# Optimization experiments

Measured on AMD Instinct MI355X. Metric: run time of the kernel, lower is better.

## Reference

```python
import jax, jax.numpy as jnp
import numpy as np

B, H, N, T, E, D = 8, 8, 64, 256, 512, 64  # batch, heads, series, window, embed, feature
TAU = 1.0
DH = E // H  # per-head dim = 64


def setup_inputs() -> dict:
    key = jax.random.key(0)
    ks = jax.random.split(key, 7)
    f32 = jnp.float32
    return {
        "q": jax.random.normal(ks[0], (B, N, E), f32),
        "k": jax.random.normal(ks[1], (B, N, E), f32),
        "v": jax.random.normal(ks[2], (B, H, N, T, D), f32),
        # nn.Linear weights use torch (out, in) convention, bias=False
        "Wq": jax.random.normal(ks[3], (E, E), f32) * (E ** -0.5),
        "Wk": jax.random.normal(ks[4], (E, E), f32) * (E ** -0.5),
        # causal-convolution temporal mixing kernel per head/series
        "Wconv": jax.random.normal(ks[5], (H, N, T, T), f32) * (T ** -0.5),
        # concat projection: (out=D, in=H*D)
        "Wcat": jax.random.normal(ks[6], (D, H * D), f32) * ((H * D) ** -0.5),
    }


def reference(q, k, v, Wq, Wk, Wconv, Wcat):
    # Q/K projections, split into heads: (B,N,E) -> (B,H,N,DH)
    Q = (q @ Wq.T).reshape(B, N, H, DH).transpose(0, 2, 1, 3)
    K = (k @ Wk.T).reshape(B, N, H, DH).transpose(0, 2, 1, 3)

    # Causal convolution V projection: lower-triangular masked temporal mixing
    causal = jnp.tril(jnp.ones((T, T), v.dtype))
    V = jnp.einsum('hnts,bhnsd->bhntd', Wconv * causal, v)  # (B,H,N,T,D)

    # tau-scaled multi-head attention over the series axis
    scores = jnp.einsum('bhid,bhjd->bhij', Q, K) / (TAU * np.sqrt(DH).astype(np.float32))
    attn = jax.nn.softmax(scores, axis=-1)  # (B,H,N,N); dropout=0 (eval)
    out = jnp.einsum('bhij,bhjtd->bhitd', attn, V)  # (B,H,N,T,D)

    # reshape/permute chain == (B,H,N,T,D) -> (B,N,T,H*D)
    out = out.transpose(0, 2, 3, 1, 4).reshape(B, N, T, H * D)
    return out @ Wcat.T  # (B,N,T,D)
```

## Files before the change

kernel.cpp:

```cpp
#include <hip/hip_runtime.h>
#include <hip/hip_bf16.h>


typedef unsigned short u16;
typedef unsigned int u32;
typedef __attribute__((ext_vector_type(8))) short short8;
typedef __attribute__((ext_vector_type(4))) float f32x4;

static __device__ __forceinline__ u16 f2bf(float f) {
    u32 x; __builtin_memcpy(&x, &f, 4);
    u32 r = (x + 0x7fffu + ((x >> 16) & 1u)) >> 16;
    return (u16)r;
}
static __device__ __forceinline__ short8 pack8(float4 a, float4 b) {
    short8 r;
    r[0] = (short)f2bf(a.x); r[1] = (short)f2bf(a.y);
    r[2] = (short)f2bf(a.z); r[3] = (short)f2bf(a.w);
    r[4] = (short)f2bf(b.x); r[5] = (short)f2bf(b.y);
    r[6] = (short)f2bf(b.z); r[7] = (short)f2bf(b.w);
    return r;
}
static __device__ __forceinline__ short8 mk_bfrag(f32x4 a, f32x4 b) {
    u32 w0 = (__float_as_uint(a[0]) >> 16) | (__float_as_uint(a[1]) & 0xffff0000u);
    u32 w1 = (__float_as_uint(a[2]) >> 16) | (__float_as_uint(a[3]) & 0xffff0000u);
    u32 w2 = (__float_as_uint(b[0]) >> 16) | (__float_as_uint(b[1]) & 0xffff0000u);
    u32 w3 = (__float_as_uint(b[2]) >> 16) | (__float_as_uint(b[3]) & 0xffff0000u);
    uint4 u = make_uint4(w0, w1, w2, w3);
    short8 r; __builtin_memcpy(&r, &u, 16); return r;
}
static __device__ __forceinline__ short8 mk_bfrag_rnd(f32x4 a, f32x4 b) {
    short8 r;
    r[0] = (short)f2bf(a[0]); r[1] = (short)f2bf(a[1]);
    r[2] = (short)f2bf(a[2]); r[3] = (short)f2bf(a[3]);
    r[4] = (short)f2bf(b[0]); r[5] = (short)f2bf(b[1]);
    r[6] = (short)f2bf(b[2]); r[7] = (short)f2bf(b[3]);
    return r;
}
static __device__ __forceinline__ uint2 pk4(f32x4 d) {
    return make_uint2((__float_as_uint(d[0]) >> 16) | (__float_as_uint(d[1]) & 0xffff0000u),
                      (__float_as_uint(d[2]) >> 16) | (__float_as_uint(d[3]) & 0xffff0000u));
}

__global__ __launch_bounds__(256) void proj_qk(
        const float* __restrict__ q, const float* __restrict__ k,
        const float* __restrict__ Wq, const float* __restrict__ Wk,
        float* __restrict__ Qh, float* __restrict__ Kh) {
    const int et = blockIdx.x, rt = blockIdx.y, z = blockIdx.z;
    const float* X = z ? k : q;
    const float* W = z ? Wk : Wq;
    float* Out = z ? Kh : Qh;
    __shared__ float Xs[32][65];
    __shared__ float Ws[32][65];
    const int tid = threadIdx.x;
    const int tx = tid & 15, ty = tid >> 4;
    const int r0 = rt * 64, e0 = et * 64;
    float acc[4][4] = {};
    for (int k0 = 0; k0 < 512; k0 += 32) {
        __syncthreads();
        #pragma unroll
        for (int rep = 0; rep < 8; ++rep) {
            int lin = rep * 256 + tid;
            int kk = lin & 31, m = lin >> 5;
            Xs[kk][m] = X[(size_t)(r0 + m) * 512 + k0 + kk];
            Ws[kk][m] = W[(size_t)(e0 + m) * 512 + k0 + kk];
        }
        __syncthreads();
        #pragma unroll 8
        for (int kk = 0; kk < 32; ++kk) {
            float a0 = Xs[kk][4 * ty + 0], a1 = Xs[kk][4 * ty + 1];
            float a2 = Xs[kk][4 * ty + 2], a3 = Xs[kk][4 * ty + 3];
            float b0 = Ws[kk][4 * tx + 0], b1 = Ws[kk][4 * tx + 1];
            float b2 = Ws[kk][4 * tx + 2], b3 = Ws[kk][4 * tx + 3];
            acc[0][0] += a0 * b0; acc[0][1] += a0 * b1; acc[0][2] += a0 * b2; acc[0][3] += a0 * b3;
            acc[1][0] += a1 * b0; acc[1][1] += a1 * b1; acc[1][2] += a1 * b2; acc[1][3] += a1 * b3;
            acc[2][0] += a2 * b0; acc[2][1] += a2 * b1; acc[2][2] += a2 * b2; acc[2][3] += a2 * b3;
            acc[3][0] += a3 * b0; acc[3][1] += a3 * b1; acc[3][2] += a3 * b2; acc[3][3] += a3 * b3;
        }
    }
    #pragma unroll
    for (int i = 0; i < 4; ++i) {
        #pragma unroll
        for (int j = 0; j < 4; ++j) {
            int r = r0 + 4 * ty + i;
            int e = e0 + 4 * tx + j;
            int b = r >> 6, n = r & 63, h = e >> 6, dh = e & 63;
            Out[(((size_t)(b * 8 + h) * 64 + n) * 64) + dh] = acc[i][j];
        }
    }
}

__global__ __launch_bounds__(256) void attn_softmax(
        const float* __restrict__ Qh, const float* __restrict__ Kh,
        u16* __restrict__ Aperm) {
    const int bh = blockIdx.x;
    const int b = bh >> 3, h = bh & 7;
    const int tid = threadIdx.x;
    __shared__ float Qt[64][64];
    __shared__ float KT[64][65];
    const size_t base = (size_t)bh * 4096;
    #pragma unroll
    for (int rep = 0; rep < 16; ++rep) {
        int lin = rep * 256 + tid;
        int r = lin >> 6, c = lin & 63;
        Qt[r][c] = Qh[base + lin];
        KT[c][r] = Kh[base + lin];
    }
    __syncthreads();
    const int w = tid >> 6, lane = tid & 63;
    const int w31 = lane & 31;
    const int slot = (w31 < 16) ? ((w31 >> 2) * 8 + (w31 & 3))
                                : (((w31 - 16) >> 2) * 8 + 4 + (w31 & 3));
    const int p = h * 64 + (lane & 32) + slot;
    for (int rr = 0; rr < 16; ++rr) {
        int i = w + 4 * rr;
        float s = 0.f;
        #pragma unroll
        for (int dd = 0; dd < 64; ++dd) s += Qt[i][dd] * KT[dd][lane];
        s *= 0.125f;
        float m = s;
        #pragma unroll
        for (int off = 32; off; off >>= 1) m = fmaxf(m, __shfl_xor(m, off));
        float e = __expf(s - m);
        float sum = e;
        #pragma unroll
        for (int off = 32; off; off >>= 1) sum += __shfl_xor(sum, off);
        Aperm[((size_t)(b * 64 + i) << 9) + p] = f2bf(e / sum);
    }
}

template<int TI, int OFF>
__device__ __forceinline__ void load_tile(short8 wc[18], const float* __restrict__ wcb,
                                          int lo, int hi) {
    const int t = TI * 16 + lo;
    #pragma unroll
    for (int kk = 0; kk <= TI / 2; ++kk) {
        const float* p = wcb + (size_t)t * 256 + kk * 32 + hi * 8;
        float4 x = ((const float4*)p)[0], y = ((const float4*)p)[1];
        float wf[8] = {x.x, x.y, x.z, x.w, y.x, y.y, y.z, y.w};
        if (kk == TI / 2) {
            int sb = kk * 32 + hi * 8;
            #pragma unroll
            for (int e = 0; e < 8; ++e)
                if (sb + e > t) wf[e] = 0.f;
        }
        short8 af;
        #pragma unroll
        for (int e = 0; e < 8; ++e) af[e] = (short)f2bf(wf[e]);
        wc[OFF + kk] = af;
    }
}

template<int W>
__device__ __forceinline__ void load_wconv_w(short8 wc[18], const float* __restrict__ wcb,
                                             int lo, int hi) {
    load_tile<2 * W,      0        >(wc, wcb, lo, hi);
    load_tile<2 * W + 1,  W + 1    >(wc, wcb, lo, hi);
    load_tile<14 - 2 * W, 2 * W + 2>(wc, wcb, lo, hi);
    load_tile<15 - 2 * W, 10 + W   >(wc, wcb, lo, hi);
}

template<int M, int OA, int OB, int TB>
__device__ __forceinline__ void pair_conv_store(const short8 wc[18],
        const u16* __restrict__ vptB, u16* __restrict__ vout,
        int lo, int hi, short8 J1, short8 J2) {
    f32x4 aA[4] = {}, aB[4] = {};
    #pragma unroll
    for (int kk = 0; kk <= M; ++kk) {
        short8 bfr[4];
        #pragma unroll
        for (int di = 0; di < 4; ++di) {
            int d = di * 16 + lo;
            int sc = kk * 4 + hi;
            bfr[di] = *(const short8*)&vptB[d * 256 + ((sc ^ (d & 7)) << 3)];
        }
        #pragma unroll
        for (int di = 0; di < 4; ++di) {
            aA[di] = __builtin_amdgcn_mfma_f32_16x16x32_bf16(wc[OA + kk], bfr[di], aA[di], 0, 0, 0);
            aB[di] = __builtin_amdgcn_mfma_f32_16x16x32_bf16(wc[OB + kk], bfr[di], aB[di], 0, 0, 0);
        }
    }
    const f32x4 z = {};
    #pragma unroll
    for (int di = 0; di < 4; ++di) {
        short8 Xc = mk_bfrag_rnd(aA[di], aB[di]);
        f32x4 D1 = __builtin_amdgcn_mfma_f32_16x16x32_bf16(Xc, J1, z, 0, 0, 0);
        f32x4 D2 = __builtin_amdgcn_mfma_f32_16x16x32_bf16(Xc, J2, z, 0, 0, 0);
        *(uint2*)&vout[(size_t)(TB + lo) * 64 + di * 16 + hi * 4] = pk4(D1);
        *(uint2*)&vout[(size_t)(TB + 16 + lo) * 64 + di * 16 + hi * 4] = pk4(D2);
    }
}

template<int W>
__device__ __forceinline__ void phaseB_w(const short8 wc[18], const u16* __restrict__ vptB,
        u16* __restrict__ vout, int lo, int hi, short8 J1, short8 J2) {
    pair_conv_store<W,     0,         W + 1,  32 * W       >(wc, vptB, vout, lo, hi, J1, J2);
    pair_conv_store<7 - W, 2 * W + 2, 10 + W, (14 - 2 * W) * 16>(wc, vptB, vout, lo, hi, J1, J2);
}

__global__ __launch_bounds__(256, 2) void conv_mfma(
        const float* __restrict__ v, const float* __restrict__ Wconv,
        const float* __restrict__ Wcat, u16* __restrict__ Vp, int b0, int bs) {
    const int split = blockIdx.x;
    const int hj = blockIdx.y, h = hj >> 6, j = hj & 63;
    const int tid = threadIdx.x;
    const int w = tid >> 6, l = tid & 63;
    const int lo = l & 15, hi = l >> 4;
    const int bstart = b0 + split * bs;
    const int blbase = split * bs;

    __shared__ u16 vptB[64 * 256];

    short8 J1, J2;
    #pragma unroll
    for (int e = 0; e < 8; ++e) {
        int pie = (e < 4) ? (hi * 4 + e) : (16 + hi * 4 + (e - 4));
        J1[e] = (pie == lo) ? (short)0x3F80 : (short)0;
        J2[e] = (pie == lo + 16) ? (short)0x3F80 : (short)0;
    }

    short8 wc[18];
    const float* wcb = Wconv + (size_t)hj * 65536;
    if (w == 0)      load_wconv_w<0>(wc, wcb, lo, hi);
    else if (w == 1) load_wconv_w<1>(wc, wcb, lo, hi);
    else if (w == 2) load_wconv_w<2>(wc, wcb, lo, hi);
    else             load_wconv_w<3>(wc, wcb, lo, hi);

    short8 wcat[2][4];
    #pragma unroll
    for (int kk = 0; kk < 2; ++kk)
        #pragma unroll
        for (int di = 0; di < 4; ++di) {
            const float* p = Wcat + (size_t)(di * 16 + lo) * 512 + h * 64 + kk * 32 + hi * 8;
            wcat[kk][di] = pack8(((const float4*)p)[0], ((const float4*)p)[1]);
        }

    for (int i = 0; i < bs; ++i) {
        const int b = bstart + i;
        __syncthreads();
        const size_t vb = ((size_t)(b * 8 + h) * 64 + j) * 16384;
        #pragma unroll
        for (int si = 0; si < 4; ++si) {
            const float* p = v + vb + (size_t)(w * 64 + si * 16 + lo) * 64;
            f32x4 a4[4] = {};
            #pragma unroll
            for (int kk = 0; kk < 2; ++kk) {
                const float4* q = (const float4*)(p + kk * 32 + hi * 8);
                short8 af = pack8(q[0], q[1]);
                #pragma unroll
                for (int di = 0; di < 4; ++di)
                    a4[di] = __builtin_amdgcn_mfma_f32_16x16x32_bf16(af, wcat[kk][di], a4[di], 0, 0, 0);
            }
            int s0 = w * 64 + si * 16 + hi * 4;
            #pragma unroll
            for (int di = 0; di < 4; ++di) {
                int d = di * 16 + lo;
                u32 lo32 = (u32)f2bf(a4[di][0]) | ((u32)f2bf(a4[di][1]) << 16);
                u32 hi32 = (u32)f2bf(a4[di][2]) | ((u32)f2bf(a4[di][3]) << 16);
                *(uint2*)&vptB[d * 256 + (((s0 >> 3) ^ (d & 7)) << 3) + (s0 & 7)] =
                    make_uint2(lo32, hi32);
            }
        }
        __syncthreads();
        u16* vout = Vp + ((size_t)(blbase + i) * 512 + hj) * 16384;
        if (w == 0)      phaseB_w<0>(wc, vptB, vout, lo, hi, J1, J2);
        else if (w == 1) phaseB_w<1>(wc, vptB, vout, lo, hi, J1, J2);
        else if (w == 2) phaseB_w<2>(wc, vptB, vout, lo, hi, J1, J2);
        else             phaseB_w<3>(wc, vptB, vout, lo, hi, J1, J2);
    }
}

__global__ __launch_bounds__(256) void final_mfma(
        const u16* __restrict__ Aperm, const u16* __restrict__ Vp,
        float* __restrict__ out, int bbase) {
    const int nblk = blockIdx.x;
    const int bl = blockIdx.y, b = bbase + bl;
    const int tid = threadIdx.x;
    const int w = tid >> 6, l = tid & 63;
    const int lo = l & 15, hi = l >> 4;
    const int nb = nblk * 128 + w * 32;

    short8 I1, I2;
    #pragma unroll
    for (int e = 0; e < 8; ++e) {
        I1[e] = (hi * 8 + e == lo) ? (short)0x3F80 : (short)0;
        I2[e] = (hi * 8 + e == lo + 16) ? (short)0x3F80 : (short)0;
    }

    const u16* ab = Aperm + ((size_t)b << 15);
    const u16* vb = Vp + (size_t)bl * 512 * 16384;

    f32x4 acc[4][2] = {};
    const f32x4 z = {};
    #pragma unroll 2
    for (int ks = 0; ks < 16; ++ks) {
        const int k0 = ks * 32;
        short8 af[4];
        #pragma unroll
        for (int mi = 0; mi < 4; ++mi)
            af[mi] = *(const short8*)&ab[(size_t)(mi * 16 + lo) * 512 + k0 + hi * 8];
        short8 X1 = *(const short8*)&vb[(size_t)(k0 + lo) * 16384 + nb + hi * 8];
        short8 X2 = *(const short8*)&vb[(size_t)(k0 + 16 + lo) * 16384 + nb + hi * 8];
        f32x4 t1a = __builtin_amdgcn_mfma_f32_16x16x32_bf16(X1, I1, z, 0, 0, 0);
        f32x4 t1b = __builtin_amdgcn_mfma_f32_16x16x32_bf16(X1, I2, z, 0, 0, 0);
        f32x4 t2a = __builtin_amdgcn_mfma_f32_16x16x32_bf16(X2, I1, z, 0, 0, 0);
        f32x4 t2b = __builtin_amdgcn_mfma_f32_16x16x32_bf16(X2, I2, z, 0, 0, 0);
        short8 B0 = mk_bfrag(t1a, t2a);
        short8 B1 = mk_bfrag(t1b, t2b);
        #pragma unroll
        for (int mi = 0; mi < 4; ++mi) {
            acc[mi][0] = __builtin_amdgcn_mfma_f32_16x16x32_bf16(af[mi], B0, acc[mi][0], 0, 0, 0);
            acc[mi][1] = __builtin_amdgcn_mfma_f32_16x16x32_bf16(af[mi], B1, acc[mi][1], 0, 0, 0);
        }
    }

    float* ob = out + ((size_t)b << 20);
    #pragma unroll
    for (int mi = 0; mi < 4; ++mi) {
        #pragma unroll
        for (int nt = 0; nt < 2; ++nt) {
            int td = nb + nt * 16 + lo;
            #pragma unroll
            for (int r = 0; r < 4; ++r) {
                int i = mi * 16 + hi * 4 + r;
                ob[(size_t)i * 16384 + td] = acc[mi][nt][r];
            }
        }
    }
}

extern "C" void kernel_launch(void* const* d_in, const int* in_sizes, int n_in,
                              void* d_out, int out_size, void* d_ws, size_t ws_size,
                              hipStream_t stream) {
    const float* q     = (const float*)d_in[0];
    const float* k     = (const float*)d_in[1];
    const float* v     = (const float*)d_in[2];
    const float* Wq    = (const float*)d_in[3];
    const float* Wk    = (const float*)d_in[4];
    const float* Wconv = (const float*)d_in[5];
    const float* Wcat  = (const float*)d_in[6];
    float* out = (float*)d_out;

    u16* Aperm = (u16*)d_ws;
    float* Qh = (float*)(Aperm + 262144);
    float* Kh = Qh + 262144;
    u16* Vp = (u16*)(Kh + 262144);
    const size_t fixed = 262144 * 2 + (size_t)2 * 262144 * 4;

    int bc = 8;
    while (bc > 1 && fixed + (size_t)bc * 512 * 16384 * 2 > ws_size) bc >>= 1;

    proj_qk<<<dim3(8, 8, 2), 256, 0, stream>>>(q, k, Wq, Wk, Qh, Kh);
    attn_softmax<<<64, 256, 0, stream>>>(Qh, Kh, Aperm);
    for (int b0 = 0; b0 < 8; b0 += bc) {
        int nsplit = (bc + 3) / 4;
        int bs = bc / nsplit;
        conv_mfma<<<dim3(nsplit, 512), 256, 0, stream>>>(v, Wconv, Wcat, Vp, b0, bs);
        final_mfma<<<dim3(128, bc), 256, 0, stream>>>(Aperm, Vp, out, b0);
    }
}
```

Baseline: 230.6 us.

## Double-buffer conv LDS, remap conv block grid, software-pipeline final GEMM loads

The conv kernel now alternates between two LDS buffers across batch iterations, which removes one barrier per iteration. It also launches a 1D grid whose index mapping interleaves the two batch splits in groups of 8, so blocks sharing the same Wconv slice run near each other. The final GEMM loop is fully unrolled with ping-pong register prefetch of the next k-step's A and V fragments, to hide global load latency behind MFMAs. In exchange, LDS use doubles (64KB per block), which may limit occupancy, and register pressure rises. The prefetch past the last step wraps to k=0, which wastes loads but is harmless.

```diff
diff --git a/kernel.cpp b/kernel.cpp
--- a/kernel.cpp
+++ b/kernel.cpp
@@ -199,16 +199,19 @@
 
 __global__ __launch_bounds__(256, 2) void conv_mfma(
         const float* __restrict__ v, const float* __restrict__ Wconv,
-        const float* __restrict__ Wcat, u16* __restrict__ Vp, int b0, int bs) {
-    const int split = blockIdx.x;
-    const int hj = blockIdx.y, h = hj >> 6, j = hj & 63;
+        const float* __restrict__ Wcat, u16* __restrict__ Vp,
+        int b0, int bs, int nsplit) {
+    const int bid = blockIdx.x;
+    const int split = (nsplit > 1) ? ((bid >> 3) & 1) : 0;
+    const int hj = (nsplit > 1) ? (((bid >> 4) << 3) | (bid & 7)) : bid;
+    const int h = hj >> 6, j = hj & 63;
     const int tid = threadIdx.x;
     const int w = tid >> 6, l = tid & 63;
     const int lo = l & 15, hi = l >> 4;
     const int bstart = b0 + split * bs;
     const int blbase = split * bs;
 
-    __shared__ u16 vptB[64 * 256];
+    __shared__ u16 vptB[2][64 * 256];
 
     short8 J1, J2;
     #pragma unroll
@@ -236,7 +239,7 @@
 
     for (int i = 0; i < bs; ++i) {
         const int b = bstart + i;
-        __syncthreads();
+        u16* buf = vptB[i & 1];
         const size_t vb = ((size_t)(b * 8 + h) * 64 + j) * 16384;
         #pragma unroll
         for (int si = 0; si < 4; ++si) {
@@ -256,16 +259,16 @@
                 int d = di * 16 + lo;
                 u32 lo32 = (u32)f2bf(a4[di][0]) | ((u32)f2bf(a4[di][1]) << 16);
                 u32 hi32 = (u32)f2bf(a4[di][2]) | ((u32)f2bf(a4[di][3]) << 16);
-                *(uint2*)&vptB[d * 256 + (((s0 >> 3) ^ (d & 7)) << 3) + (s0 & 7)] =
+                *(uint2*)&buf[d * 256 + (((s0 >> 3) ^ (d & 7)) << 3) + (s0 & 7)] =
                     make_uint2(lo32, hi32);
             }
         }
         __syncthreads();
         u16* vout = Vp + ((size_t)(blbase + i) * 512 + hj) * 16384;
-        if (w == 0)      phaseB_w<0>(wc, vptB, vout, lo, hi, J1, J2);
-        else if (w == 1) phaseB_w<1>(wc, vptB, vout, lo, hi, J1, J2);
-        else if (w == 2) phaseB_w<2>(wc, vptB, vout, lo, hi, J1, J2);
-        else             phaseB_w<3>(wc, vptB, vout, lo, hi, J1, J2);
+        if (w == 0)      phaseB_w<0>(wc, buf, vout, lo, hi, J1, J2);
+        else if (w == 1) phaseB_w<1>(wc, buf, vout, lo, hi, J1, J2);
+        else if (w == 2) phaseB_w<2>(wc, buf, vout, lo, hi, J1, J2);
+        else             phaseB_w<3>(wc, buf, vout, lo, hi, J1, J2);
     }
 }
 
@@ -291,27 +294,41 @@
 
     f32x4 acc[4][2] = {};
     const f32x4 z = {};
-    #pragma unroll 2
-    for (int ks = 0; ks < 16; ++ks) {
-        const int k0 = ks * 32;
-        short8 af[4];
-        #pragma unroll
-        for (int mi = 0; mi < 4; ++mi)
-            af[mi] = *(const short8*)&ab[(size_t)(mi * 16 + lo) * 512 + k0 + hi * 8];
-        short8 X1 = *(const short8*)&vb[(size_t)(k0 + lo) * 16384 + nb + hi * 8];
-        short8 X2 = *(const short8*)&vb[(size_t)(k0 + 16 + lo) * 16384 + nb + hi * 8];
-        f32x4 t1a = __builtin_amdgcn_mfma_f32_16x16x32_bf16(X1, I1, z, 0, 0, 0);
-        f32x4 t1b = __builtin_amdgcn_mfma_f32_16x16x32_bf16(X1, I2, z, 0, 0, 0);
-        f32x4 t2a = __builtin_amdgcn_mfma_f32_16x16x32_bf16(X2, I1, z, 0, 0, 0);
-        f32x4 t2b = __builtin_amdgcn_mfma_f32_16x16x32_bf16(X2, I2, z, 0, 0, 0);
-        short8 B0 = mk_bfrag(t1a, t2a);
-        short8 B1 = mk_bfrag(t1b, t2b);
-        #pragma unroll
-        for (int mi = 0; mi < 4; ++mi) {
-            acc[mi][0] = __builtin_amdgcn_mfma_f32_16x16x32_bf16(af[mi], B0, acc[mi][0], 0, 0, 0);
-            acc[mi][1] = __builtin_amdgcn_mfma_f32_16x16x32_bf16(af[mi], B1, acc[mi][1], 0, 0, 0);
-        }
-    }
+
+    #define LDAF(af, k0) { \
+        _Pragma("unroll") \
+        for (int mi = 0; mi < 4; ++mi) \
+            af[mi] = *(const short8*)&ab[(size_t)(mi * 16 + lo) * 512 + (k0) + hi * 8]; }
+    #define LDX(X1, X2, k0) { \
+        X1 = *(const short8*)&vb[(size_t)((k0) + lo) * 16384 + nb + hi * 8]; \
+        X2 = *(const short8*)&vb[(size_t)((k0) + 16 + lo) * 16384 + nb + hi * 8]; }
+    #define COMPUTE(af, X1, X2) { \
+        f32x4 t1a = __builtin_amdgcn_mfma_f32_16x16x32_bf16(X1, I1, z, 0, 0, 0); \
+        f32x4 t1b = __builtin_amdgcn_mfma_f32_16x16x32_bf16(X1, I2, z, 0, 0, 0); \
+        f32x4 t2a = __builtin_amdgcn_mfma_f32_16x16x32_bf16(X2, I1, z, 0, 0, 0); \
+        f32x4 t2b = __builtin_amdgcn_mfma_f32_16x16x32_bf16(X2, I2, z, 0, 0, 0); \
+        short8 B0 = mk_bfrag(t1a, t2a); \
+        short8 B1 = mk_bfrag(t1b, t2b); \
+        _Pragma("unroll") \
+        for (int mi = 0; mi < 4; ++mi) { \
+            acc[mi][0] = __builtin_amdgcn_mfma_f32_16x16x32_bf16(af[mi], B0, acc[mi][0], 0, 0, 0); \
+            acc[mi][1] = __builtin_amdgcn_mfma_f32_16x16x32_bf16(af[mi], B1, acc[mi][1], 0, 0, 0); \
+        } }
+
+    short8 afA[4], afB[4], X1A, X2A, X1B, X2B;
+    LDAF(afA, 0); LDX(X1A, X2A, 0);
+    #pragma unroll
+    for (int ks = 0; ks < 16; ks += 2) {
+        const int k1 = (ks + 1) * 32;
+        const int k2 = ((ks + 2) & 15) * 32;
+        LDAF(afB, k1); LDX(X1B, X2B, k1);
+        COMPUTE(afA, X1A, X2A);
+        LDAF(afA, k2); LDX(X1A, X2A, k2);
+        COMPUTE(afB, X1B, X2B);
+    }
+    #undef LDAF
+    #undef LDX
+    #undef COMPUTE
 
     float* ob = out + ((size_t)b << 20);
     #pragma unroll
@@ -354,7 +371,7 @@
     for (int b0 = 0; b0 < 8; b0 += bc) {
         int nsplit = (bc + 3) / 4;
         int bs = bc / nsplit;
-        conv_mfma<<<dim3(nsplit, 512), 256, 0, stream>>>(v, Wconv, Wcat, Vp, b0, bs);
+        conv_mfma<<<dim3(nsplit * 512), 256, 0, stream>>>(v, Wconv, Wcat, Vp, b0, bs, nsplit);
         final_mfma<<<dim3(128, bc), 256, 0, stream>>>(Aperm, Vp, out, b0);
     }
 }
```

After: 226.2 us. About the same (-1.9%).
